# Kernel tuning notes

Measured on AMD Instinct MI355X. Metric: run time of the kernel, lower is better.

Reference implementation:

```python
import jax, jax.numpy as jnp
import numpy as np

V, E, H, B, S, T, OOV = 50000, 128, 256, 32, 400, 16, 20


def setup_inputs() -> dict:
    key = jax.random.key(0)
    ks = jax.random.split(key, 20)
    def p(i, shape, s=0.02):
        return jax.random.normal(ks[i], shape, dtype=jnp.float32) * s
    z = lambda *shape: jnp.zeros(shape, dtype=jnp.float32)
    return {
        'input_seq': jax.random.randint(ks[0], (B, S), 0, V),
        'input_seq_ext': jax.random.randint(ks[1], (B, S), 0, V + OOV),
        'target_seq': jax.random.randint(ks[2], (B, T), 0, V),
        'embedding': p(3, (V, E)),
        'enc_Wih_f': p(4, (3 * H, E)), 'enc_Whh_f': p(5, (3 * H, H)),
        'enc_bih_f': z(3 * H), 'enc_bhh_f': z(3 * H),
        'enc_Wih_b': p(6, (3 * H, E)), 'enc_Whh_b': p(7, (3 * H, H)),
        'enc_bih_b': z(3 * H), 'enc_bhh_b': z(3 * H),
        'proj_W': p(8, (H, 2 * H)), 'proj_b': z(H),
        'bridge_W': p(9, (H, 2 * H)), 'bridge_b': z(H),
        'dec_Wih': p(10, (3 * H, E + 2 * H)), 'dec_Whh': p(11, (3 * H, H)),
        'dec_bih': z(3 * H), 'dec_bhh': z(3 * H),
        'attn_Wq': p(12, (H, H)), 'attn_We': p(13, (1, H)),
        'lin_W': p(14, (H, E + 3 * H)), 'lin_b': z(H),
        'pgen_W': p(15, (1, E + 3 * H)), 'pgen_b': z(1),
        'out_W': p(16, (V, H)), 'out_b': z(V),
    }


def gru_cell(x, h, Wih, Whh, bih, bhh):
    # PyTorch GRU cell math
    gi = x @ Wih.T + bih
    gh = h @ Whh.T + bhh
    ir, iz, inn = jnp.split(gi, 3, axis=-1)
    hr, hz, hn = jnp.split(gh, 3, axis=-1)
    r = jax.nn.sigmoid(ir + hr)
    zg = jax.nn.sigmoid(iz + hz)
    n = jnp.tanh(inn + r * hn)
    return (1.0 - zg) * n + zg * h


def run_gru(xs, h0, Wih, Whh, bih, bhh):
    def step(h, x):
        h2 = gru_cell(x, h, Wih, Whh, bih, bhh)
        return h2, h2
    hT, hs = jax.lax.scan(step, h0, xs)
    return hs, hT


def reference(input_seq, input_seq_ext, target_seq, embedding,
              enc_Wih_f, enc_Whh_f, enc_bih_f, enc_bhh_f,
              enc_Wih_b, enc_Whh_b, enc_bih_b, enc_bhh_b,
              proj_W, proj_b, bridge_W, bridge_b,
              dec_Wih, dec_Whh, dec_bih, dec_bhh,
              attn_Wq, attn_We, lin_W, lin_b,
              pgen_W, pgen_b, out_W, out_b):
    Bsz, Slen = input_seq.shape
    Tlen = target_seq.shape[1]
    Hd = bridge_W.shape[0]
    dt = embedding.dtype

    # ---- encoder (bidirectional GRU) ----
    emb_src = embedding[input_seq].transpose(1, 0, 2)  # (S,B,E)
    h0e = jnp.zeros((Bsz, Hd), dt)
    hs_f, hf = run_gru(emb_src, h0e, enc_Wih_f, enc_Whh_f, enc_bih_f, enc_bhh_f)
    hs_b_rev, hb = run_gru(emb_src[::-1], h0e, enc_Wih_b, enc_Whh_b, enc_bih_b, enc_bhh_b)
    enc_states = jnp.concatenate([hs_f, hs_b_rev[::-1]], axis=-1)  # (S,B,2H)
    proj = enc_states @ proj_W.T + proj_b                           # (S,B,H)
    h = jnp.tanh(jnp.concatenate([hf, hb], axis=-1) @ bridge_W.T + bridge_b)  # (B,H)

    rows = jnp.arange(Bsz)
    toks = target_seq[:, :Tlen - 1].T  # teacher forcing, (T-1,B)

    def dec_step(h, tok):
        e = embedding[tok]                                            # (B,E)
        scores = jnp.tanh(h @ attn_Wq.T + proj) @ attn_We[0]          # (S,B)
        alphas = jax.nn.softmax(scores, axis=0)                       # softmax over seq dim
        context = jnp.einsum('sb,sbd->bd', alphas, enc_states)        # (B,2H)
        h2 = gru_cell(jnp.concatenate([e, context], axis=-1), h,
                      dec_Wih, dec_Whh, dec_bih, dec_bhh)             # (B,H)
        cat = jnp.concatenate([e, h2, context], axis=-1)              # (B,E+3H)
        p_gen = jax.nn.sigmoid(cat @ pgen_W.T + pgen_b)               # (B,1)
        logits = (cat @ lin_W.T + lin_b) @ out_W.T + out_b            # (B,V)
        gen = p_gen * jax.nn.softmax(logits, axis=-1)
        attn = (1.0 - p_gen) * alphas.T                               # (B,S)
        ext = jnp.concatenate([gen, jnp.zeros((Bsz, OOV), dt)], axis=-1) + 1e-12
        ext = ext.at[rows[:, None], input_seq_ext].add(attn)          # scatter_add copy dist
        return h2, jnp.log(ext)

    _, outs = jax.lax.scan(dec_step, h, toks)                         # (T-1,B,V+OOV)
    out0 = jnp.zeros((1,) + outs.shape[1:], outs.dtype)               # t=0 row stays zero
    return jnp.concatenate([out0, outs], axis=0)                      # (T,B,V+OOV)
```

## Files before the change

kernel.cpp:

```cpp
#include <hip/hip_runtime.h>

#define SLEN 400
#define BATCH 32
#define TLEN 16
#define NDEC 15
#define EDIM 128
#define HDIM 256
#define H3 768
#define VVOC 50000
#define VEXT 50020
#define SCHUNK 50

__device__ __forceinline__ float frcp(float x){ return __builtin_amdgcn_rcpf(x); }
__device__ __forceinline__ float fsig(float x){ return frcp(1.f + __expf(-x)); }
__device__ __forceinline__ float ftanh(float x){
  float e = __expf(2.f*x);
  return 1.f - 2.f*frcp(e + 1.f);
}

typedef _Float16 h2 __attribute__((ext_vector_type(2)));
typedef _Float16 half8 __attribute__((ext_vector_type(8)));
typedef float floatx4 __attribute__((ext_vector_type(4)));

__device__ __forceinline__ h2 u2h(unsigned u){ return __builtin_bit_cast(h2, u); }
__device__ __forceinline__ unsigned pkh(float a, float b){
  h2 v; v.x=(_Float16)a; v.y=(_Float16)b;
  return __builtin_bit_cast(unsigned, v);
}

#if __has_builtin(__builtin_amdgcn_fdot2)
__device__ __forceinline__ float fdot2h(h2 a, h2 b, float c){
  return __builtin_amdgcn_fdot2(a, b, c, false);
}
#else
__device__ __forceinline__ float fdot2h(h2 a, h2 b, float c){
  return fmaf((float)a.x,(float)b.x, fmaf((float)a.y,(float)b.y, c));
}
#endif

__device__ __forceinline__ float wred_sum(float v){
  #pragma unroll
  for (int o=32;o>0;o>>=1) v += __shfl_down(v,o,64);
  return v;
}
__device__ __forceinline__ float wred_max(float v){
  #pragma unroll
  for (int o=32;o>0;o>>=1) v = fmaxf(v, __shfl_down(v,o,64));
  return v;
}
__device__ __forceinline__ float block_max(float v, float* red){
  v = wred_max(v);
  int lane = threadIdx.x & 63, wid = threadIdx.x >> 6;
  if (!lane) red[wid] = v;
  __syncthreads();
  if (threadIdx.x == 0){
    float m = red[0];
    int nw = blockDim.x >> 6;
    for (int w=1;w<nw;++w) m = fmaxf(m, red[w]);
    red[0] = m;
  }
  __syncthreads();
  v = red[0];
  __syncthreads();
  return v;
}
__device__ __forceinline__ float block_sum(float v, float* red){
  v = wred_sum(v);
  int lane = threadIdx.x & 63, wid = threadIdx.x >> 6;
  if (!lane) red[wid] = v;
  __syncthreads();
  if (threadIdx.x == 0){
    float m = red[0];
    int nw = blockDim.x >> 6;
    for (int w=1;w<nw;++w) m += red[w];
    red[0] = m;
  }
  __syncthreads();
  v = red[0];
  __syncthreads();
  return v;
}

__global__ __launch_bounds__(64) void k_embed(
    const int* __restrict__ input_seq, const int* __restrict__ target_seq,
    const float* __restrict__ embedding,
    _Float16* __restrict__ emb16, float* __restrict__ cat_all, _Float16* __restrict__ cat16)
{
  int row = blockIdx.x;
  if (row < SLEN*BATCH) {
    int s = row >> 5, b = row & 31;
    int tok = input_seq[b*SLEN + s];
    float2 v = ((const float2*)(embedding + (size_t)tok*EDIM))[threadIdx.x];
    ((unsigned*)(emb16 + (size_t)row*EDIM))[threadIdx.x] = pkh(v.x, v.y);
  } else {
    int rr = row - SLEN*BATCH;
    int t = rr >> 5, b = rr & 31;
    int tok = target_seq[b*TLEN + t];
    float2 v = ((const float2*)(embedding + (size_t)tok*EDIM))[threadIdx.x];
    ((float2*)(cat_all + (size_t)rr*896))[threadIdx.x] = v;
    ((unsigned*)(cat16 + (size_t)rr*896))[threadIdx.x] = pkh(v.x, v.y);
  }
}

__global__ __launch_bounds__(256) void k_cvtv5(
    const float* __restrict__ S0, _Float16* __restrict__ D0, int n0,
    const float* __restrict__ S1, _Float16* __restrict__ D1, int n1,
    const float* __restrict__ S2, _Float16* __restrict__ D2, int n2,
    const float* __restrict__ S3, _Float16* __restrict__ D3, int n3,
    const float* __restrict__ S4, _Float16* __restrict__ D4, int n4)
{
  const float* S; _Float16* D; int n8;
  switch (blockIdx.y){
    case 0: S=S0; D=D0; n8=n0; break;
    case 1: S=S1; D=D1; n8=n1; break;
    case 2: S=S2; D=D2; n8=n2; break;
    case 3: S=S3; D=D3; n8=n3; break;
    default: S=S4; D=D4; n8=n4; break;
  }
  int i = blockIdx.x*256 + threadIdx.x;
  if (i >= n8) return;
  float4 a = ((const float4*)S)[i*2];
  float4 b = ((const float4*)S)[i*2+1];
  uint4 o;
  o.x = pkh(a.x,a.y); o.y = pkh(a.z,a.w);
  o.z = pkh(b.x,b.y); o.w = pkh(b.z,b.w);
  ((uint4*)D)[i] = o;
}

__global__ __launch_bounds__(256) void k_cvtv(
    const float* __restrict__ S, _Float16* __restrict__ D, int n8)
{
  int i = blockIdx.x*256 + threadIdx.x;
  if (i >= n8) return;
  float4 a = ((const float4*)S)[i*2];
  float4 b = ((const float4*)S)[i*2+1];
  uint4 o;
  o.x = pkh(a.x,a.y); o.y = pkh(a.z,a.w);
  o.z = pkh(b.x,b.y); o.w = pkh(b.z,b.w);
  ((uint4*)D)[i] = o;
}

__global__ __launch_bounds__(64) void k_cvtk5(
    const float* __restrict__ W0, uint4* __restrict__ D0,
    const float* __restrict__ W1, uint4* __restrict__ D1,
    const float* __restrict__ W2, uint4* __restrict__ D2,
    const float* __restrict__ W3, uint4* __restrict__ D3,
    const float* __restrict__ W4, uint4* __restrict__ D4)
{
  const float* W; uint4* D; int ldw, coloff, nrows, nk8;
  switch (blockIdx.y){
    case 0: W=W0; D=D0; ldw=HDIM; coloff=0;   nrows=H3;   nk8=32; break;
    case 1: W=W1; D=D1; ldw=HDIM; coloff=0;   nrows=H3;   nk8=32; break;
    case 2: W=W2; D=D2; ldw=640;  coloff=128; nrows=H3;   nk8=64; break;
    case 3: W=W3; D=D3; ldw=HDIM; coloff=0;   nrows=H3;   nk8=32; break;
    default: W=W4; D=D4; ldw=HDIM; coloff=0;  nrows=HDIM; nk8=32; break;
  }
  int row = blockIdx.x, k8 = threadIdx.x;
  if (row >= nrows || k8 >= nk8) return;
  const float* s = W + (size_t)row*ldw + coloff + k8*8;
  float4 x = *(const float4*)s;
  float4 y = *(const float4*)(s+4);
  uint4 o;
  o.x = pkh(x.x,x.y); o.y = pkh(x.z,x.w);
  o.z = pkh(y.x,y.y); o.w = pkh(y.z,y.w);
  D[(size_t)k8*nrows + row] = o;
}

__global__ __launch_bounds__(256) void k_gmm(
    const _Float16* __restrict__ A, int lda,
    const _Float16* __restrict__ W, int ldw,
    const float* __restrict__ bias,
    float* __restrict__ C, _Float16* __restrict__ C16, int ldc,
    int M, int N, int K, int rev)
{
  __shared__ __align__(16) _Float16 Al[128*64];
  __shared__ __align__(16) _Float16 Wl[128*64];
  int tid = threadIdx.x;
  int wv = tid >> 6, l = tid & 63;
  int wr = (wv>>1)*64, wc = (wv&1)*64;
  int lr = l & 15, lh = l >> 4;
  int m0 = blockIdx.y*128, n0 = blockIdx.x*128;
  floatx4 acc[4][4];
  #pragma unroll
  for (int i=0;i<4;++i)
    #pragma unroll
    for (int jn=0;jn<4;++jn) acc[i][jn] = (floatx4){0.f,0.f,0.f,0.f};

  for (int kc=0; kc<K; kc+=64){
    #pragma unroll
    for (int i=0;i<4;++i){
      int idx = tid + i*256;
      int row = idx>>3, c = idx&7;
      int m = m0+row;
      uint4 v = {0u,0u,0u,0u};
      if (m < M){
        int am = m;
        if (rev){ int s = m>>5; am = ((SLEN-1-s)<<5)|(m&31); }
        v = *(const uint4*)&A[(size_t)am*lda + kc + c*8];
      }
      *(uint4*)&Al[row*64 + ((c ^ (row&7))<<3)] = v;
    }
    #pragma unroll
    for (int i=0;i<4;++i){
      int idx = tid + i*256;
      int row = idx>>3, c = idx&7;
      int n = n0+row;
      uint4 v = {0u,0u,0u,0u};
      if (n < N) v = *(const uint4*)&W[(size_t)n*ldw + kc + c*8];
      *(uint4*)&Wl[row*64 + ((c ^ (row&7))<<3)] = v;
    }
    __syncthreads();
    #pragma unroll
    for (int ks=0; ks<2; ++ks){
      half8 af0, af1, af2, af3, bf0, bf1, bf2, bf3;
      {
        int c = ks*4 + lh;
        int r0 = wr + 0*16 + lr, r1 = wr + 1*16 + lr, r2 = wr + 2*16 + lr, r3 = wr + 3*16 + lr;
        af0 = *(const half8*)&Al[r0*64 + ((c ^ (r0&7))<<3)];
        af1 = *(const half8*)&Al[r1*64 + ((c ^ (r1&7))<<3)];
        af2 = *(const half8*)&Al[r2*64 + ((c ^ (r2&7))<<3)];
        af3 = *(const half8*)&Al[r3*64 + ((c ^ (r3&7))<<3)];
        int n0l = wc + 0*16 + lr, n1l = wc + 1*16 + lr, n2l = wc + 2*16 + lr, n3l = wc + 3*16 + lr;
        bf0 = *(const half8*)&Wl[n0l*64 + ((c ^ (n0l&7))<<3)];
        bf1 = *(const half8*)&Wl[n1l*64 + ((c ^ (n1l&7))<<3)];
        bf2 = *(const half8*)&Wl[n2l*64 + ((c ^ (n2l&7))<<3)];
        bf3 = *(const half8*)&Wl[n3l*64 + ((c ^ (n3l&7))<<3)];
      }
      half8 afs[4] = {af0, af1, af2, af3};
      half8 bfs[4] = {bf0, bf1, bf2, bf3};
      #pragma unroll
      for (int mi=0;mi<4;++mi)
        #pragma unroll
        for (int ni=0;ni<4;++ni)
          acc[mi][ni] = __builtin_amdgcn_mfma_f32_16x16x32_f16(afs[mi], bfs[ni], acc[mi][ni], 0,0,0);
    }
    __syncthreads();
  }
  #pragma unroll
  for (int mi=0;mi<4;++mi){
    #pragma unroll
    for (int q=0;q<4;++q){
      int m = m0 + wr + mi*16 + lh*4 + q;
      if (m < M){
        #pragma unroll
        for (int ni=0;ni<4;++ni){
          int n = n0 + wc + ni*16 + lr;
          if (n < N){
            float v = acc[mi][ni][q] + bias[n];
            if (C)   C[(size_t)m*ldc + n] = v;
            if (C16) C16[(size_t)m*ldc + n] = (_Float16)v;
          }
        }
      }
    }
  }
}

#define R20(M) M(0) M(1) M(2) M(3) M(4) M(5) M(6) M(7) M(8) M(9) \
               M(10) M(11) M(12) M(13) M(14) M(15) M(16) M(17) M(18) M(19)

__global__ __launch_bounds__(768) void k_enc(
    const float* __restrict__ gi_f, const float* __restrict__ gi_b,
    const uint4* __restrict__ W16_f, const uint4* __restrict__ W16_b,
    const float* __restrict__ bhh_f, const float* __restrict__ bhh_b,
    _Float16* __restrict__ enc16, float* __restrict__ hfin)
{
  int dir = blockIdx.x >> 5, b = blockIdx.x & 31;
  int jj = threadIdx.x;
  const float* gi  = dir ? gi_b  : gi_f;
  const uint4* Wp  = (dir ? W16_b : W16_f) + jj;
  float bh = (dir ? bhh_b : bhh_f)[jj];

  __shared__ __align__(16) unsigned hpk[HDIM/2];
  __shared__ __align__(16) float st[H3];
  __shared__ uint4 Wlds[12][H3];

  #pragma unroll
  for (int k8=0;k8<12;++k8) Wlds[k8][jj] = Wp[k8*H3];

#define DW(i) uint4 q##i = Wp[(12+(i))*H3];
  R20(DW)
#undef DW

  if (jj < HDIM/2) hpk[jj] = 0u;
  float hreg = 0.f;
  _Float16* dst = enc16 + (size_t)b*2*HDIM + dir*HDIM + jj;
  __syncthreads();

  for (int s=0;s<SLEN;++s){
    const float* grow = gi + ((size_t)s*BATCH + b)*H3;
    float g1 = 0.f, g2 = 0.f;
    if (jj < 512)  g1 = grow[jj];
    if (jj < HDIM) g2 = grow[2*HDIM + jj];
    float ac0=0.f, ac1=0.f, ac2=0.f, ac3=0.f;
    #pragma unroll
    for (int k8=0;k8<12;++k8){
      uint4 w = Wlds[k8][jj];
      uint4 hq = *(const uint4*)&hpk[k8*4];
      ac0 = fdot2h(u2h(w.x),u2h(hq.x),ac0);
      ac1 = fdot2h(u2h(w.y),u2h(hq.y),ac1);
      ac2 = fdot2h(u2h(w.z),u2h(hq.z),ac2);
      ac3 = fdot2h(u2h(w.w),u2h(hq.w),ac3);
    }
#define DU(i) { uint4 hq = *(const uint4*)&hpk[(12+(i))*4]; \
    ac0 = fdot2h(u2h(q##i.x),u2h(hq.x),ac0); \
    ac1 = fdot2h(u2h(q##i.y),u2h(hq.y),ac1); \
    ac2 = fdot2h(u2h(q##i.z),u2h(hq.z),ac2); \
    ac3 = fdot2h(u2h(q##i.w),u2h(hq.w),ac3); }
    R20(DU)
#undef DU
    float acc = (ac0+ac1)+(ac2+ac3) + bh;
    st[jj] = (jj < 512) ? (acc + g1) : acc;
    __syncthreads();
    if (jj < HDIM){
      float rr = fsig(st[jj]);
      float zz = fsig(st[HDIM + jj]);
      float nn = ftanh(g2 + rr*st[2*HDIM + jj]);
      float h2v = nn + zz*(hreg - nn);
      hreg = h2v;
      int srow = dir ? (SLEN-1-s) : s;
      dst[(size_t)srow*BATCH*2*HDIM] = (_Float16)h2v;
      ((_Float16*)hpk)[jj] = (_Float16)h2v;
      if (s == SLEN-1) hfin[(size_t)(dir*BATCH + b)*HDIM + jj] = h2v;
    }
    __syncthreads();
  }
}

__global__ __launch_bounds__(256) void k_bridge(
    const float* __restrict__ hfin,
    const float* __restrict__ bridge_W, const float* __restrict__ bridge_b,
    float* __restrict__ h_out)
{
  int b = blockIdx.x, j = threadIdx.x;
  __shared__ float hcat[2*HDIM];
  hcat[j]        = hfin[(size_t)b*HDIM + j];
  hcat[HDIM + j] = hfin[(size_t)(BATCH + b)*HDIM + j];
  __syncthreads();
  const float* w = bridge_W + (size_t)j*2*HDIM;
  float4 a = {0.f,0.f,0.f,0.f};
  #pragma unroll 4
  for (int k=0;k<2*HDIM;k+=4){
    float4 h4 = *(const float4*)&hcat[k];
    float4 w4 = *(const float4*)&w[k];
    a.x=fmaf(h4.x,w4.x,a.x); a.y=fmaf(h4.y,w4.y,a.y);
    a.z=fmaf(h4.z,w4.z,a.z); a.w=fmaf(h4.w,w4.w,a.w);
  }
  h_out[b*HDIM+j] = ftanh((a.x+a.y)+(a.z+a.w) + bridge_b[j]);
}

__global__ __launch_bounds__(256) void k_attnB(
    int t,
    const _Float16* __restrict__ proj16,
    const _Float16* __restrict__ enc16,
    const uint4* __restrict__ Wq16k,
    const float* __restrict__ attn_We,
    const float* __restrict__ hin,
    float* __restrict__ alphas_e,
    float* __restrict__ sum_part,
    float* __restrict__ ctx_part)
{
  int ch = blockIdx.x, b = blockIdx.y;
  int tid = threadIdx.x;
  __shared__ float q_s[HDIM], we_s[HDIM], sc[SCHUNK], red[8];
  __shared__ __align__(16) unsigned hq[HDIM/2];

  we_s[tid] = attn_We[tid];
  if (tid < HDIM/2){
    float2 hv = *(const float2*)&hin[b*HDIM + tid*2];
    hq[tid] = pkh(hv.x, hv.y);
  }
  __syncthreads();
  {
    float a0=0.f,a1=0.f,a2=0.f,a3=0.f;
    #pragma unroll
    for (int k8=0;k8<32;++k8){
      uint4 w = Wq16k[(size_t)k8*HDIM + tid];
      uint4 hp = *(const uint4*)&hq[k8*4];
      a0 = fdot2h(u2h(w.x),u2h(hp.x),a0);
      a1 = fdot2h(u2h(w.y),u2h(hp.y),a1);
      a2 = fdot2h(u2h(w.z),u2h(hp.z),a2);
      a3 = fdot2h(u2h(w.w),u2h(hp.w),a3);
    }
    q_s[tid] = (a0+a1)+(a2+a3);
  }
  __syncthreads();
  {
    int wave = tid >> 6, lane = tid & 63;
    int d0 = lane*4;
    float4 qv = *(const float4*)&q_s[d0];
    float4 wv = *(const float4*)&we_s[d0];
    for (int is = wave; is < SCHUNK; is += 4){
      int s = ch*SCHUNK + is;
      uint2 p = *(const uint2*)&proj16[((size_t)(s*BATCH + b))*HDIM + d0];
      h2 pa = u2h(p.x), pb = u2h(p.y);
      float v = ftanh(qv.x+(float)pa.x)*wv.x + ftanh(qv.y+(float)pa.y)*wv.y
              + ftanh(qv.z+(float)pb.x)*wv.z + ftanh(qv.w+(float)pb.y)*wv.w;
      v = wred_sum(v);
      if (lane == 0){
        float e = __expf(v);
        sc[is] = e;
        alphas_e[((size_t)t*SLEN + s)*BATCH + b] = e;
      }
    }
  }
  __syncthreads();
  {
    float sv = (tid < SCHUNK) ? sc[tid] : 0.f;
    sv = block_sum(sv, red);
    if (tid == 0) sum_part[b*8 + ch] = sv;
  }
  {
    float a0=0.f, a1=0.f;
    for (int is=0; is<SCHUNK; ++is){
      int s = ch*SCHUNK + is;
      unsigned u = *(const unsigned*)&enc16[((size_t)(s*BATCH + b) << 9) + tid*2];
      h2 ev = u2h(u);
      float e = sc[is];
      a0 = fmaf(e, (float)ev.x, a0);
      a1 = fmaf(e, (float)ev.y, a1);
    }
    float2 o; o.x = a0; o.y = a1;
    *(float2*)&ctx_part[(((size_t)b*8 + ch) << 9) + tid*2] = o;
  }
}

__global__ __launch_bounds__(256) void k_gruD(
    int t,
    const float* __restrict__ ctx_part,
    const float* __restrict__ sum_part,
    const float* __restrict__ gie_all,
    const uint4* __restrict__ dWck16,
    const uint4* __restrict__ dWhk16,
    const float* __restrict__ dec_bhh,
    const float* __restrict__ hin,
    float* __restrict__ hout,
    float* __restrict__ cat_all, _Float16* __restrict__ cat16,
    float* __restrict__ sums_all)
{
  int ch = blockIdx.x, b = blockIdx.y;
  int tid = threadIdx.x;
  int jl = tid & 31, slice = tid >> 5;
  __shared__ __align__(16) unsigned cpk[HDIM], hpk[HDIM/2];
  __shared__ float hf[HDIM];
  __shared__ float pc[3][8][32], ph[3][8][32];
  __shared__ float invs;

  if (tid == 0){
    float ssum = 0.f;
    #pragma unroll
    for (int c=0;c<8;++c) ssum += sum_part[b*8 + c];
    float inv = 1.f/ssum;
    invs = inv;
    if (ch == 0) sums_all[t*BATCH + b] = inv;
  }
  if (tid < HDIM/2){
    float2 hv = *(const float2*)&hin[b*HDIM + tid*2];
    hpk[tid] = pkh(hv.x, hv.y);
    hf[tid*2] = hv.x; hf[tid*2+1] = hv.y;
  }
  __syncthreads();
  {
    int d0 = tid*2;
    float c0=0.f, c1=0.f;
    #pragma unroll
    for (int c=0;c<8;++c){
      float2 v = *(const float2*)&ctx_part[(((size_t)b*8 + c) << 9) + d0];
      c0 += v.x; c1 += v.y;
    }
    c0 *= invs; c1 *= invs;
    cpk[tid] = pkh(c0, c1);
    if (ch == 0){
      int r = t*BATCH + b;
      cat_all[(size_t)r*896 + 384 + d0]     = c0;
      cat_all[(size_t)r*896 + 384 + d0 + 1] = c1;
      cat16[(size_t)r*896 + 384 + d0]     = (_Float16)c0;
      cat16[(size_t)r*896 + 384 + d0 + 1] = (_Float16)c1;
    }
  }
  __syncthreads();
  {
    int jb = ch*32 + jl;
    float c0=0.f,c1=0.f,c2=0.f, g0=0.f,g1=0.f,g2=0.f;
    #pragma unroll
    for (int i=0;i<8;++i){
      int k8 = slice*8 + i;
      uint4 hq = *(const uint4*)&cpk[k8*4];
      uint4 w0 = dWck16[(size_t)k8*H3 + jb];
      uint4 w1 = dWck16[(size_t)k8*H3 + 256 + jb];
      uint4 w2 = dWck16[(size_t)k8*H3 + 512 + jb];
      c0 = fdot2h(u2h(w0.x),u2h(hq.x),c0); c0 = fdot2h(u2h(w0.y),u2h(hq.y),c0);
      c0 = fdot2h(u2h(w0.z),u2h(hq.z),c0); c0 = fdot2h(u2h(w0.w),u2h(hq.w),c0);
      c1 = fdot2h(u2h(w1.x),u2h(hq.x),c1); c1 = fdot2h(u2h(w1.y),u2h(hq.y),c1);
      c1 = fdot2h(u2h(w1.z),u2h(hq.z),c1); c1 = fdot2h(u2h(w1.w),u2h(hq.w),c1);
      c2 = fdot2h(u2h(w2.x),u2h(hq.x),c2); c2 = fdot2h(u2h(w2.y),u2h(hq.y),c2);
      c2 = fdot2h(u2h(w2.z),u2h(hq.z),c2); c2 = fdot2h(u2h(w2.w),u2h(hq.w),c2);
    }
    #pragma unroll
    for (int i=0;i<4;++i){
      int k8 = slice*4 + i;
      uint4 hq = *(const uint4*)&hpk[k8*4];
      uint4 w0 = dWhk16[(size_t)k8*H3 + jb];
      uint4 w1 = dWhk16[(size_t)k8*H3 + 256 + jb];
      uint4 w2 = dWhk16[(size_t)k8*H3 + 512 + jb];
      g0 = fdot2h(u2h(w0.x),u2h(hq.x),g0); g0 = fdot2h(u2h(w0.y),u2h(hq.y),g0);
      g0 = fdot2h(u2h(w0.z),u2h(hq.z),g0); g0 = fdot2h(u2h(w0.w),u2h(hq.w),g0);
      g1 = fdot2h(u2h(w1.x),u2h(hq.x),g1); g1 = fdot2h(u2h(w1.y),u2h(hq.y),g1);
      g1 = fdot2h(u2h(w1.z),u2h(hq.z),g1); g1 = fdot2h(u2h(w1.w),u2h(hq.w),g1);
      g2 = fdot2h(u2h(w2.x),u2h(hq.x),g2); g2 = fdot2h(u2h(w2.y),u2h(hq.y),g2);
      g2 = fdot2h(u2h(w2.z),u2h(hq.z),g2); g2 = fdot2h(u2h(w2.w),u2h(hq.w),g2);
    }
    pc[0][slice][jl]=c0; pc[1][slice][jl]=c1; pc[2][slice][jl]=c2;
    ph[0][slice][jl]=g0; ph[1][slice][jl]=g1; ph[2][slice][jl]=g2;
  }
  __syncthreads();
  if (tid < 32){
    int j = tid, r = t*BATCH + b;
    int jj = ch*32 + j;
    float gi0 = gie_all[(size_t)r*H3 + jj];
    float gi1 = gie_all[(size_t)r*H3 + 256 + jj];
    float gi2 = gie_all[(size_t)r*H3 + 512 + jj];
    float gh0 = dec_bhh[jj], gh1 = dec_bhh[256 + jj], gh2 = dec_bhh[512 + jj];
    #pragma unroll
    for (int c=0;c<8;++c){
      gi0 += pc[0][c][j]; gi1 += pc[1][c][j]; gi2 += pc[2][c][j];
      gh0 += ph[0][c][j]; gh1 += ph[1][c][j]; gh2 += ph[2][c][j];
    }
    float rr = fsig(gi0 + gh0);
    float zz = fsig(gi1 + gh1);
    float nn = ftanh(gi2 + rr*gh2);
    float hp = hf[jj];
    float h2v = nn + zz*(hp - nn);
    hout[b*HDIM + jj] = h2v;
    cat_all[(size_t)r*896 + 128 + jj] = h2v;
    cat16[(size_t)r*896 + 128 + jj] = (_Float16)h2v;
  }
}

__global__ __launch_bounds__(64) void k_pgen(
    const float* __restrict__ cat_all,
    const float* __restrict__ pgen_W, const float* __restrict__ pgen_b,
    float* __restrict__ pgen_all)
{
  int r = blockIdx.x;
  const float* c = cat_all + (size_t)r*896;
  float acc = 0.f;
  for (int k=threadIdx.x; k<896; k+=64) acc = fmaf(c[k], pgen_W[k], acc);
  acc = wred_sum(acc);
  if (threadIdx.x==0) pgen_all[r] = fsig(acc + pgen_b[0]);
}

__global__ __launch_bounds__(256) void k_rowred(
    const _Float16* __restrict__ logits,
    float* __restrict__ row_max, float* __restrict__ row_sum)
{
  int r = blockIdx.x;
  const uint4* row = (const uint4*)(logits + (size_t)r*VVOC);
  __shared__ float red[8];
  float m = -1e30f;
  for (int v=threadIdx.x; v<VVOC/8; v+=256){
    uint4 x = row[v];
    h2 a=u2h(x.x), bb=u2h(x.y), c=u2h(x.z), d=u2h(x.w);
    float m1 = fmaxf(fmaxf((float)a.x,(float)a.y), fmaxf((float)bb.x,(float)bb.y));
    float m2 = fmaxf(fmaxf((float)c.x,(float)c.y), fmaxf((float)d.x,(float)d.y));
    m = fmaxf(m, fmaxf(m1,m2));
  }
  m = block_max(m, red);
  float s = 0.f;
  for (int v=threadIdx.x; v<VVOC/8; v+=256){
    uint4 x = row[v];
    h2 a=u2h(x.x), bb=u2h(x.y), c=u2h(x.z), d=u2h(x.w);
    s += __expf((float)a.x-m) + __expf((float)a.y-m) + __expf((float)bb.x-m) + __expf((float)bb.y-m)
       + __expf((float)c.x-m) + __expf((float)c.y-m) + __expf((float)d.x-m) + __expf((float)d.y-m);
  }
  s = block_sum(s, red);
  if (threadIdx.x==0){ row_max[r]=m; row_sum[r]=1.f/s; }
}

__global__ __launch_bounds__(256) void k_final(
    const _Float16* __restrict__ logits, const float* __restrict__ pgen_all,
    const float* __restrict__ row_max, const float* __restrict__ row_sum,
    float* __restrict__ out)
{
  int v = blockIdx.x*256 + threadIdx.x;
  if (v >= VEXT) return;
  int b = blockIdx.y, t = blockIdx.z;
  size_t o = ((size_t)t*BATCH + b)*VEXT + v;
  if (t == 0){ out[o] = 0.f; return; }
  int r = (t-1)*BATCH + b;
  float val = 1e-12f;
  if (v < VVOC)
    val += pgen_all[r] * row_sum[r] * __expf((float)logits[(size_t)r*VVOC + v] - row_max[r]);
  out[o] = val;
}

__global__ __launch_bounds__(512) void k_scatter(
    const int* __restrict__ input_seq_ext,
    const float* __restrict__ alphas_e, const float* __restrict__ sums_all,
    const float* __restrict__ pgen_all,
    float* __restrict__ out)
{
  int r = blockIdx.x;
  int s = threadIdx.x;
  if (s >= SLEN) return;
  int t = r >> 5, b = r & 31;
  float w = (1.f - pgen_all[r]) * alphas_e[((size_t)t*SLEN + s)*BATCH + b] * sums_all[r];
  int idx = input_seq_ext[b*SLEN + s];
  atomicAdd(&out[((size_t)(t+1)*BATCH + b)*VEXT + idx], w);
}

__global__ __launch_bounds__(256) void k_log(float* __restrict__ out)
{
  int v = blockIdx.x*256 + threadIdx.x;
  if (v >= VEXT) return;
  int b = blockIdx.y, t = blockIdx.z + 1;
  size_t o = ((size_t)t*BATCH + b)*VEXT + v;
  out[o] = __logf(out[o]);
}

extern "C" void kernel_launch(void* const* d_in, const int* in_sizes, int n_in,
                              void* d_out, int out_size, void* d_ws, size_t ws_size,
                              hipStream_t stream)
{
  (void)in_sizes; (void)n_in; (void)out_size; (void)ws_size;
  const int*   input_seq     = (const int*)d_in[0];
  const int*   input_seq_ext = (const int*)d_in[1];
  const int*   target_seq    = (const int*)d_in[2];
  const float* embedding     = (const float*)d_in[3];
  const float* enc_Wih_f     = (const float*)d_in[4];
  const float* enc_Whh_f     = (const float*)d_in[5];
  const float* enc_bih_f     = (const float*)d_in[6];
  const float* enc_bhh_f     = (const float*)d_in[7];
  const float* enc_Wih_b     = (const float*)d_in[8];
  const float* enc_Whh_b     = (const float*)d_in[9];
  const float* enc_bih_b     = (const float*)d_in[10];
  const float* enc_bhh_b     = (const float*)d_in[11];
  const float* proj_W        = (const float*)d_in[12];
  const float* proj_b        = (const float*)d_in[13];
  const float* bridge_W      = (const float*)d_in[14];
  const float* bridge_b      = (const float*)d_in[15];
  const float* dec_Wih       = (const float*)d_in[16];
  const float* dec_Whh       = (const float*)d_in[17];
  const float* dec_bih       = (const float*)d_in[18];
  const float* dec_bhh       = (const float*)d_in[19];
  const float* attn_Wq       = (const float*)d_in[20];
  const float* attn_We       = (const float*)d_in[21];
  const float* lin_W         = (const float*)d_in[22];
  const float* lin_b         = (const float*)d_in[23];
  const float* pgen_W        = (const float*)d_in[24];
  const float* pgen_b        = (const float*)d_in[25];
  const float* out_W         = (const float*)d_in[26];
  const float* out_b         = (const float*)d_in[27];
  float* out = (float*)d_out;
  float* ws  = (float*)d_ws;

  _Float16* emb16    = (_Float16*)(ws + 0);
  _Float16* Wih16_f  = (_Float16*)(ws + 409600);
  _Float16* Wih16_b  = (_Float16*)(ws + 458752);
  _Float16* proj_W16 = (_Float16*)(ws + 507904);
  _Float16* lin_W16  = (_Float16*)(ws + 573440);
  _Float16* cat16    = (_Float16*)(ws + 688128);
  _Float16* lin16    = (_Float16*)(ws + 903168);
  _Float16* dWih16   = (_Float16*)(ws + 964608);
  _Float16* enc16    = (_Float16*)(ws + 1638400);
  float* hfin        = ws + 4915200;
  _Float16* proj16   = (_Float16*)(ws + 8192000);
  float* gi_f        = ws + 11468800;
  float* gi_b        = ws + 21299200;
  _Float16* logits16 = (_Float16*)(ws + 11468800);
  _Float16* out_W16  = (_Float16*)(ws + 23468800);
  uint4* Wq16k       = (uint4*)(ws + 33145600);
  uint4* dWck16      = (uint4*)(ws + 33178368);
  uint4* dWhk16      = (uint4*)(ws + 33374976);
  float* ctx_part    = ws + 33473280;
  float* sum_part    = ws + 33604352;
  float* sums_all    = ws + 33604608;
  float* hbuf0       = ws + 33605088;
  float* hbuf1       = ws + 33613280;
  uint4* W16_f       = (uint4*)(ws + 35000000);
  uint4* W16_b       = (uint4*)(ws + 35098304);
  float* cat_all     = ws + 35468800;
  float* gie_all     = ws + 35898880;
  float* alphas_e    = ws + 36275712;
  float* pgen_all    = ws + 36467712;
  float* row_max     = ws + 36468192;
  float* row_sum     = ws + 36468672;

  k_embed<<<dim3(SLEN*BATCH + NDEC*BATCH), dim3(64), 0, stream>>>(
      input_seq, target_seq, embedding, emb16, cat_all, cat16);

  k_cvtv5<<<dim3(240, 5), dim3(256), 0, stream>>>(
      enc_Wih_f, Wih16_f, 12288,
      enc_Wih_b, Wih16_b, 12288,
      proj_W,    proj_W16, 16384,
      lin_W,     lin_W16,  28672,
      dec_Wih,   dWih16,   61440);
  k_cvtk5<<<dim3(H3, 5), dim3(64), 0, stream>>>(
      enc_Whh_f, W16_f,
      enc_Whh_b, W16_b,
      dec_Wih,   dWck16,
      dec_Whh,   dWhk16,
      attn_Wq,   Wq16k);

  k_gmm<<<dim3(6,100), dim3(256), 0, stream>>>(emb16, EDIM, Wih16_f, EDIM, enc_bih_f,
      gi_f, (_Float16*)nullptr, H3, SLEN*BATCH, H3, EDIM, 0);
  k_gmm<<<dim3(6,100), dim3(256), 0, stream>>>(emb16, EDIM, Wih16_b, EDIM, enc_bih_b,
      gi_b, (_Float16*)nullptr, H3, SLEN*BATCH, H3, EDIM, 1);

  k_enc<<<dim3(64), dim3(768), 0, stream>>>(gi_f, gi_b, W16_f, W16_b, enc_bhh_f, enc_bhh_b,
      enc16, hfin);

  k_cvtv<<<dim3((12800000/8+255)/256), dim3(256), 0, stream>>>(out_W, out_W16, 12800000/8);

  k_gmm<<<dim3(2,100), dim3(256), 0, stream>>>(enc16, 2*HDIM, proj_W16, 2*HDIM, proj_b,
      (float*)nullptr, proj16, HDIM, SLEN*BATCH, HDIM, 2*HDIM, 0);

  k_bridge<<<dim3(BATCH), dim3(256), 0, stream>>>(hfin, bridge_W, bridge_b, hbuf0);

  k_gmm<<<dim3(6,4), dim3(256), 0, stream>>>(cat16, 896, dWih16, 640, dec_bih,
      gie_all, (_Float16*)nullptr, H3, NDEC*BATCH, H3, EDIM, 0);

  float* hb[2] = {hbuf0, hbuf1};
  for (int t=0;t<NDEC;++t){
    k_attnB<<<dim3(8,32), dim3(256), 0, stream>>>(t, proj16, enc16, Wq16k, attn_We,
        hb[t&1], alphas_e, sum_part, ctx_part);
    k_gruD<<<dim3(8,32), dim3(256), 0, stream>>>(t, ctx_part, sum_part, gie_all,
        dWck16, dWhk16, dec_bhh, hb[t&1], hb[(t+1)&1], cat_all, cat16, sums_all);
  }

  k_gmm<<<dim3(2,4), dim3(256), 0, stream>>>(cat16, 896, lin_W16, 896, lin_b,
      (float*)nullptr, lin16, HDIM, NDEC*BATCH, HDIM, 896, 0);
  k_pgen<<<dim3(NDEC*BATCH), dim3(64), 0, stream>>>(cat_all, pgen_W, pgen_b, pgen_all);
  k_gmm<<<dim3(391,4), dim3(256), 0, stream>>>(lin16, HDIM, out_W16, HDIM, out_b,
      (float*)nullptr, logits16, VVOC, NDEC*BATCH, VVOC, HDIM, 0);
  k_rowred<<<dim3(NDEC*BATCH), dim3(256), 0, stream>>>(logits16, row_max, row_sum);
  k_final<<<dim3(196, BATCH, TLEN), dim3(256), 0, stream>>>(logits16, pgen_all, row_max, row_sum, out);
  k_scatter<<<dim3(NDEC*BATCH), dim3(512), 0, stream>>>(input_seq_ext, alphas_e, sums_all, pgen_all, out);
  k_log<<<dim3(196, BATCH, NDEC), dim3(256), 0, stream>>>(out);
}
```

Measured before the change: 1.176 ms.

## Quantize encoder recurrent weights to FP8, store gates in fp16, fuse output passes

Twenty of the 32 k-chunks of the encoder recurrent weights were held in registers as fp16. They now become scaled e4m3 FP8 values loaded from global memory each step and dotted against an fp32 copy of the hidden state, which is meant to cut register pressure in the serial encoder loop. The input-gate activations are stored as fp16 instead of fp32, halving their traffic. The output stage drops the row-max pass and fuses the final write with the log: the output is zeroed with a memset, the copy distribution is scattered, and one kernel then adds the softmax term and takes the log. Skipping the max subtraction risks overflow for large logits, and FP8 weights reduce accuracy.

```diff
diff --git a/kernel.cpp b/kernel.cpp
--- a/kernel.cpp
+++ b/kernel.cpp
@@ -21,6 +21,7 @@
 typedef _Float16 h2 __attribute__((ext_vector_type(2)));
 typedef _Float16 half8 __attribute__((ext_vector_type(8)));
 typedef float floatx4 __attribute__((ext_vector_type(4)));
+typedef float floatx2 __attribute__((ext_vector_type(2)));
 
 __device__ __forceinline__ h2 u2h(unsigned u){ return __builtin_bit_cast(h2, u); }
 __device__ __forceinline__ unsigned pkh(float a, float b){
@@ -38,30 +39,40 @@
 }
 #endif
 
+#if __has_builtin(__builtin_amdgcn_cvt_pk_f32_fp8)
+template<bool HI>
+__device__ __forceinline__ floatx2 fp8pk2f(unsigned u){
+  return __builtin_amdgcn_cvt_pk_f32_fp8(u, HI);
+}
+#else
+__device__ __forceinline__ float e4m3f(unsigned b){
+  unsigned s=b>>7, e=(b>>3)&15, m=b&7;
+  float v = e ? exp2f((float)e-7.f)*(1.f+0.125f*m) : 0.001953125f*m;
+  return s ? -v : v;
+}
+template<bool HI>
+__device__ __forceinline__ floatx2 fp8pk2f(unsigned u){
+  unsigned x = HI ? (u>>16) : u;
+  floatx2 r; r.x = e4m3f(x & 0xFF); r.y = e4m3f((x>>8)&0xFF);
+  return r;
+}
+#endif
+
+__device__ __forceinline__ unsigned f32_to_e4m3(float v){
+  float a = fabsf(v); unsigned s = (v<0.f)?0x80u:0u;
+  if (!(a > 0.f)) return s;
+  if (a < 0.015625f){ int m = (int)(a*512.f + 0.5f); if (m>7) return s|8u; return s|(unsigned)m; }
+  int e = (int)floorf(log2f(a));
+  float mant = a*exp2f((float)-e) - 1.f;
+  int m = (int)(mant*8.f + 0.5f);
+  if (m==8){ m=0; e+=1; }
+  if (e > 8){ e=8; m=6; }
+  return s | (unsigned)((e+7)<<3) | (unsigned)m;
+}
+
 __device__ __forceinline__ float wred_sum(float v){
   #pragma unroll
   for (int o=32;o>0;o>>=1) v += __shfl_down(v,o,64);
-  return v;
-}
-__device__ __forceinline__ float wred_max(float v){
-  #pragma unroll
-  for (int o=32;o>0;o>>=1) v = fmaxf(v, __shfl_down(v,o,64));
-  return v;
-}
-__device__ __forceinline__ float block_max(float v, float* red){
-  v = wred_max(v);
-  int lane = threadIdx.x & 63, wid = threadIdx.x >> 6;
-  if (!lane) red[wid] = v;
-  __syncthreads();
-  if (threadIdx.x == 0){
-    float m = red[0];
-    int nw = blockDim.x >> 6;
-    for (int w=1;w<nw;++w) m = fmaxf(m, red[w]);
-    red[0] = m;
-  }
-  __syncthreads();
-  v = red[0];
-  __syncthreads();
   return v;
 }
 __device__ __forceinline__ float block_sum(float v, float* red){
@@ -164,6 +175,25 @@
   o.x = pkh(x.x,x.y); o.y = pkh(x.z,x.w);
   o.z = pkh(y.x,y.y); o.w = pkh(y.z,y.w);
   D[(size_t)k8*nrows + row] = o;
+}
+
+__global__ __launch_bounds__(32) void k_cvt8(
+    const float* __restrict__ Wf, uint2* __restrict__ Df,
+    const float* __restrict__ Wb, uint2* __restrict__ Db)
+{
+  int row = blockIdx.x;
+  const float* W = blockIdx.y ? Wb : Wf;
+  uint2* D = blockIdx.y ? Db : Df;
+  int i = threadIdx.x;
+  if (i >= 20) return;
+  const float* s = W + (size_t)row*HDIM + (12+i)*8;
+  unsigned lo = 0, hi = 0;
+  #pragma unroll
+  for (int k=0;k<4;++k) lo |= f32_to_e4m3(s[k]*64.f) << (8*k);
+  #pragma unroll
+  for (int k=0;k<4;++k) hi |= f32_to_e4m3(s[4+k]*64.f) << (8*k);
+  uint2 o; o.x = lo; o.y = hi;
+  D[(size_t)i*H3 + row] = o;
 }
 
 __global__ __launch_bounds__(256) void k_gmm(
@@ -256,42 +286,39 @@
   }
 }
 
-#define R20(M) M(0) M(1) M(2) M(3) M(4) M(5) M(6) M(7) M(8) M(9) \
-               M(10) M(11) M(12) M(13) M(14) M(15) M(16) M(17) M(18) M(19)
-
 __global__ __launch_bounds__(768) void k_enc(
-    const float* __restrict__ gi_f, const float* __restrict__ gi_b,
+    const _Float16* __restrict__ gi16_f, const _Float16* __restrict__ gi16_b,
     const uint4* __restrict__ W16_f, const uint4* __restrict__ W16_b,
+    const uint2* __restrict__ W8_f, const uint2* __restrict__ W8_b,
     const float* __restrict__ bhh_f, const float* __restrict__ bhh_b,
     _Float16* __restrict__ enc16, float* __restrict__ hfin)
 {
   int dir = blockIdx.x >> 5, b = blockIdx.x & 31;
   int jj = threadIdx.x;
-  const float* gi  = dir ? gi_b  : gi_f;
+  const _Float16* gi = dir ? gi16_b : gi16_f;
   const uint4* Wp  = (dir ? W16_b : W16_f) + jj;
+  const uint2* W8p = (dir ? W8_b  : W8_f ) + jj;
   float bh = (dir ? bhh_b : bhh_f)[jj];
 
   __shared__ __align__(16) unsigned hpk[HDIM/2];
+  __shared__ __align__(16) float hf[HDIM];
   __shared__ __align__(16) float st[H3];
   __shared__ uint4 Wlds[12][H3];
 
   #pragma unroll
   for (int k8=0;k8<12;++k8) Wlds[k8][jj] = Wp[k8*H3];
 
-#define DW(i) uint4 q##i = Wp[(12+(i))*H3];
-  R20(DW)
-#undef DW
-
   if (jj < HDIM/2) hpk[jj] = 0u;
+  if (jj < HDIM)   hf[jj] = 0.f;
   float hreg = 0.f;
   _Float16* dst = enc16 + (size_t)b*2*HDIM + dir*HDIM + jj;
   __syncthreads();
 
   for (int s=0;s<SLEN;++s){
-    const float* grow = gi + ((size_t)s*BATCH + b)*H3;
+    const _Float16* grow = gi + ((size_t)s*BATCH + b)*H3;
     float g1 = 0.f, g2 = 0.f;
-    if (jj < 512)  g1 = grow[jj];
-    if (jj < HDIM) g2 = grow[2*HDIM + jj];
+    if (jj < 512)  g1 = (float)grow[jj];
+    if (jj < HDIM) g2 = (float)grow[2*HDIM + jj];
     float ac0=0.f, ac1=0.f, ac2=0.f, ac3=0.f;
     #pragma unroll
     for (int k8=0;k8<12;++k8){
@@ -302,14 +329,21 @@
       ac2 = fdot2h(u2h(w.z),u2h(hq.z),ac2);
       ac3 = fdot2h(u2h(w.w),u2h(hq.w),ac3);
     }
-#define DU(i) { uint4 hq = *(const uint4*)&hpk[(12+(i))*4]; \
-    ac0 = fdot2h(u2h(q##i.x),u2h(hq.x),ac0); \
-    ac1 = fdot2h(u2h(q##i.y),u2h(hq.y),ac1); \
-    ac2 = fdot2h(u2h(q##i.z),u2h(hq.z),ac2); \
-    ac3 = fdot2h(u2h(q##i.w),u2h(hq.w),ac3); }
-    R20(DU)
-#undef DU
-    float acc = (ac0+ac1)+(ac2+ac3) + bh;
+    float as0=0.f, as1=0.f, as2=0.f, as3=0.f;
+    #pragma unroll
+    for (int i=0;i<20;++i){
+      uint2 p = W8p[(size_t)i*H3];
+      int k0 = (12+i)*8;
+      float4 ha = *(const float4*)&hf[k0];
+      float4 hb = *(const float4*)&hf[k0+4];
+      floatx2 w01 = fp8pk2f<false>(p.x), w23 = fp8pk2f<true>(p.x);
+      floatx2 w45 = fp8pk2f<false>(p.y), w67 = fp8pk2f<true>(p.y);
+      as0 = fmaf(w01.x,ha.x, fmaf(w01.y,ha.y, as0));
+      as1 = fmaf(w23.x,ha.z, fmaf(w23.y,ha.w, as1));
+      as2 = fmaf(w45.x,hb.x, fmaf(w45.y,hb.y, as2));
+      as3 = fmaf(w67.x,hb.z, fmaf(w67.y,hb.w, as3));
+    }
+    float acc = (ac0+ac1)+(ac2+ac3) + ((as0+as1)+(as2+as3))*0.015625f + bh;
     st[jj] = (jj < 512) ? (acc + g1) : acc;
     __syncthreads();
     if (jj < HDIM){
@@ -321,6 +355,7 @@
       int srow = dir ? (SLEN-1-s) : s;
       dst[(size_t)srow*BATCH*2*HDIM] = (_Float16)h2v;
       ((_Float16*)hpk)[jj] = (_Float16)h2v;
+      hf[jj] = h2v;
       if (s == SLEN-1) hfin[(size_t)(dir*BATCH + b)*HDIM + jj] = h2v;
     }
     __syncthreads();
@@ -550,48 +585,21 @@
   if (threadIdx.x==0) pgen_all[r] = fsig(acc + pgen_b[0]);
 }
 
-__global__ __launch_bounds__(256) void k_rowred(
-    const _Float16* __restrict__ logits,
-    float* __restrict__ row_max, float* __restrict__ row_sum)
+__global__ __launch_bounds__(256) void k_rowsum(
+    const _Float16* __restrict__ logits, float* __restrict__ row_sum)
 {
   int r = blockIdx.x;
   const uint4* row = (const uint4*)(logits + (size_t)r*VVOC);
   __shared__ float red[8];
-  float m = -1e30f;
-  for (int v=threadIdx.x; v<VVOC/8; v+=256){
-    uint4 x = row[v];
-    h2 a=u2h(x.x), bb=u2h(x.y), c=u2h(x.z), d=u2h(x.w);
-    float m1 = fmaxf(fmaxf((float)a.x,(float)a.y), fmaxf((float)bb.x,(float)bb.y));
-    float m2 = fmaxf(fmaxf((float)c.x,(float)c.y), fmaxf((float)d.x,(float)d.y));
-    m = fmaxf(m, fmaxf(m1,m2));
-  }
-  m = block_max(m, red);
   float s = 0.f;
   for (int v=threadIdx.x; v<VVOC/8; v+=256){
     uint4 x = row[v];
     h2 a=u2h(x.x), bb=u2h(x.y), c=u2h(x.z), d=u2h(x.w);
-    s += __expf((float)a.x-m) + __expf((float)a.y-m) + __expf((float)bb.x-m) + __expf((float)bb.y-m)
-       + __expf((float)c.x-m) + __expf((float)c.y-m) + __expf((float)d.x-m) + __expf((float)d.y-m);
+    s += __expf((float)a.x) + __expf((float)a.y) + __expf((float)bb.x) + __expf((float)bb.y)
+       + __expf((float)c.x) + __expf((float)c.y) + __expf((float)d.x) + __expf((float)d.y);
   }
   s = block_sum(s, red);
-  if (threadIdx.x==0){ row_max[r]=m; row_sum[r]=1.f/s; }
-}
-
-__global__ __launch_bounds__(256) void k_final(
-    const _Float16* __restrict__ logits, const float* __restrict__ pgen_all,
-    const float* __restrict__ row_max, const float* __restrict__ row_sum,
-    float* __restrict__ out)
-{
-  int v = blockIdx.x*256 + threadIdx.x;
-  if (v >= VEXT) return;
-  int b = blockIdx.y, t = blockIdx.z;
-  size_t o = ((size_t)t*BATCH + b)*VEXT + v;
-  if (t == 0){ out[o] = 0.f; return; }
-  int r = (t-1)*BATCH + b;
-  float val = 1e-12f;
-  if (v < VVOC)
-    val += pgen_all[r] * row_sum[r] * __expf((float)logits[(size_t)r*VVOC + v] - row_max[r]);
-  out[o] = val;
+  if (threadIdx.x==0) row_sum[r] = 1.f/s;
 }
 
 __global__ __launch_bounds__(512) void k_scatter(
@@ -609,20 +617,27 @@
   atomicAdd(&out[((size_t)(t+1)*BATCH + b)*VEXT + idx], w);
 }
 
-__global__ __launch_bounds__(256) void k_log(float* __restrict__ out)
+__global__ __launch_bounds__(256) void k_final2(
+    const _Float16* __restrict__ logits, const float* __restrict__ pgen_all,
+    const float* __restrict__ row_sum,
+    float* __restrict__ out)
 {
   int v = blockIdx.x*256 + threadIdx.x;
   if (v >= VEXT) return;
   int b = blockIdx.y, t = blockIdx.z + 1;
   size_t o = ((size_t)t*BATCH + b)*VEXT + v;
-  out[o] = __logf(out[o]);
+  int r = (t-1)*BATCH + b;
+  float val = out[o] + 1e-12f;
+  if (v < VVOC)
+    val += pgen_all[r] * row_sum[r] * __expf((float)logits[(size_t)r*VVOC + v]);
+  out[o] = __logf(val);
 }
 
 extern "C" void kernel_launch(void* const* d_in, const int* in_sizes, int n_in,
                               void* d_out, int out_size, void* d_ws, size_t ws_size,
                               hipStream_t stream)
 {
-  (void)in_sizes; (void)n_in; (void)out_size; (void)ws_size;
+  (void)in_sizes; (void)n_in; (void)ws_size;
   const int*   input_seq     = (const int*)d_in[0];
   const int*   input_seq_ext = (const int*)d_in[1];
   const int*   target_seq    = (const int*)d_in[2];
@@ -665,8 +680,8 @@
   _Float16* enc16    = (_Float16*)(ws + 1638400);
   float* hfin        = ws + 4915200;
   _Float16* proj16   = (_Float16*)(ws + 8192000);
-  float* gi_f        = ws + 11468800;
-  float* gi_b        = ws + 21299200;
+  _Float16* gi16_f   = (_Float16*)(ws + 11468800);
+  _Float16* gi16_b   = (_Float16*)(ws + 16384000);
   _Float16* logits16 = (_Float16*)(ws + 11468800);
   _Float16* out_W16  = (_Float16*)(ws + 23468800);
   uint4* Wq16k       = (uint4*)(ws + 33145600);
@@ -677,14 +692,17 @@
   float* sums_all    = ws + 33604608;
   float* hbuf0       = ws + 33605088;
   float* hbuf1       = ws + 33613280;
+  uint2* W8_f        = (uint2*)(ws + 33621472);
+  uint2* W8_b        = (uint2*)(ws + 33652192);
   uint4* W16_f       = (uint4*)(ws + 35000000);
   uint4* W16_b       = (uint4*)(ws + 35098304);
   float* cat_all     = ws + 35468800;
   float* gie_all     = ws + 35898880;
   float* alphas_e    = ws + 36275712;
   float* pgen_all    = ws + 36467712;
-  float* row_max     = ws + 36468192;
-  float* row_sum     = ws + 36468672;
+  float* row_sum     = ws + 36468192;
+
+  (void)hipMemsetAsync(out, 0, (size_t)out_size*sizeof(float), stream);
 
   k_embed<<<dim3(SLEN*BATCH + NDEC*BATCH), dim3(64), 0, stream>>>(
       input_seq, target_seq, embedding, emb16, cat_all, cat16);
@@ -701,14 +719,15 @@
       dec_Wih,   dWck16,
       dec_Whh,   dWhk16,
       attn_Wq,   Wq16k);
+  k_cvt8<<<dim3(H3, 2), dim3(32), 0, stream>>>(enc_Whh_f, W8_f, enc_Whh_b, W8_b);
 
   k_gmm<<<dim3(6,100), dim3(256), 0, stream>>>(emb16, EDIM, Wih16_f, EDIM, enc_bih_f,
-      gi_f, (_Float16*)nullptr, H3, SLEN*BATCH, H3, EDIM, 0);
+      (float*)nullptr, gi16_f, H3, SLEN*BATCH, H3, EDIM, 0);
   k_gmm<<<dim3(6,100), dim3(256), 0, stream>>>(emb16, EDIM, Wih16_b, EDIM, enc_bih_b,
-      gi_b, (_Float16*)nullptr, H3, SLEN*BATCH, H3, EDIM, 1);
-
-  k_enc<<<dim3(64), dim3(768), 0, stream>>>(gi_f, gi_b, W16_f, W16_b, enc_bhh_f, enc_bhh_b,
-      enc16, hfin);
+      (float*)nullptr, gi16_b, H3, SLEN*BATCH, H3, EDIM, 1);
+
+  k_enc<<<dim3(64), dim3(768), 0, stream>>>(gi16_f, gi16_b, W16_f, W16_b, W8_f, W8_b,
+      enc_bhh_f, enc_bhh_b, enc16, hfin);
 
   k_cvtv<<<dim3((12800000/8+255)/256), dim3(256), 0, stream>>>(out_W, out_W16, 12800000/8);
 
@@ -733,8 +752,7 @@
   k_pgen<<<dim3(NDEC*BATCH), dim3(64), 0, stream>>>(cat_all, pgen_W, pgen_b, pgen_all);
   k_gmm<<<dim3(391,4), dim3(256), 0, stream>>>(lin16, HDIM, out_W16, HDIM, out_b,
       (float*)nullptr, logits16, VVOC, NDEC*BATCH, VVOC, HDIM, 0);
-  k_rowred<<<dim3(NDEC*BATCH), dim3(256), 0, stream>>>(logits16, row_max, row_sum);
-  k_final<<<dim3(196, BATCH, TLEN), dim3(256), 0, stream>>>(logits16, pgen_all, row_max, row_sum, out);
+  k_rowsum<<<dim3(NDEC*BATCH), dim3(256), 0, stream>>>(logits16, row_sum);
   k_scatter<<<dim3(NDEC*BATCH), dim3(512), 0, stream>>>(input_seq_ext, alphas_e, sums_all, pgen_all, out);
-  k_log<<<dim3(196, BATCH, NDEC), dim3(256), 0, stream>>>(out);
-}
+  k_final2<<<dim3(196, BATCH, NDEC), dim3(256), 0, stream>>>(logits16, pgen_all, row_sum, out);
+}
```

New measurement: 2.186 ms. 1.86x slower.
